# Kernel tuning notes

Hardware: AMD Instinct MI355X
Metric: run time of the kernel (lower is better)

The kernel has to match this reference:

```python
import jax, jax.numpy as jnp
import numpy as np

B = 16      # number of graphs (equal-sized, batch = repeat(arange(B), N))


def _knn_edges(pos, k, total):
    """Batch-aware kNN graph, torch_geometric knn_graph semantics.

    loop=False, flow='source_to_target': for each query node i, its k nearest
    neighbors j produce edges (row=j neighbor/source, col=i query/target).
    Returns (row, col) as flat global int32 index arrays of length B*N*k.
    """
    N = total // B
    posb = pos.reshape(B, N, -1)                      # [B, N, 3]
    sq = jnp.sum(posb * posb, axis=-1)                # [B, N]
    # squared Euclidean distances, [B, N, N]
    d2 = sq[:, :, None] + sq[:, None, :] - 2.0 * jnp.einsum('bnd,bmd->bnm', posb, posb)
    d2 = jnp.where(jnp.eye(N, dtype=bool)[None], jnp.inf, d2)  # exclude self-loops
    _, nbr = jax.lax.top_k(-d2, k)                    # [B, N, k] local neighbor idx
    offs = (jnp.arange(B, dtype=nbr.dtype) * N)[:, None, None]
    row = (nbr + offs).reshape(-1)                                      # neighbors (sources)
    col = jnp.broadcast_to(jnp.arange(N, dtype=nbr.dtype)[None, :, None] + offs,
                           (B, N, k)).reshape(-1)                       # query nodes (targets)
    return row, col


def reference(x, pos, batch, k):
    total = x.shape[0]
    row, col = _knn_edges(pos, k, total)
    # scatter_mean(x[col], row, dim_size=total): mean of gathered features per row index
    sums = jax.ops.segment_sum(x[col], row, num_segments=total)          # [total, d]
    cnt = jax.ops.segment_sum(jnp.ones(row.shape, x.dtype), row, num_segments=total)
    x_neigh_mean = sums / jnp.maximum(cnt, 1.0)[:, None]                 # empty rows -> 0
    return jnp.sum(jnp.abs(x - x_neigh_mean), axis=-1)                   # L1 norm, [total]


def setup_inputs() -> dict:
    key = jax.random.key(0)
    k1, k2 = jax.random.split(key)
    N = 4096
    x = jax.random.normal(k1, (B * N, 64), dtype=jnp.float32)
    pos = jax.random.normal(k2, (B * N, 3), dtype=jnp.float32)
    batch = jnp.repeat(jnp.arange(B, dtype=jnp.int64), N)
    return {"x": x, "pos": pos, "batch": batch, "k": 10}
```

## Files before the change

kernel.cpp:

```cpp
#include <hip/hip_runtime.h>
#include <stdint.h>

#define NB 16
#define NN 4096
#define KK 10
#define NL 11
#define FD 64
#define TOTAL (NB * NN)
#define NW 8
#define CH 512
#define SOCT 32
#define QG 64
#define WCAP 24
#define WPITCH 25

#define INFF __int_as_float(0x7f800000)

typedef float f2 __attribute__((ext_vector_type(2)));

__device__ __forceinline__ f2 FdP(f2 cx, f2 cy, f2 cz, f2 cq,
                                  f2 vx2, f2 vy2, f2 vz2, f2 sqi2) {
#pragma clang fp contract(fast)
    f2 t = sqi2 + cq;
    t = vx2 * cx + t;
    t = vy2 * cy + t;
    t = vz2 * cz + t;
    return t;
}

__device__ __forceinline__ uint32_t d2exact(float mx, float my, float mz, float sqi,
                                            float cx, float cy, float cz, float cw) {
    float dot = __fadd_rn(__fadd_rn(__fmul_rn(mx, cx), __fmul_rn(my, cy)),
                          __fmul_rn(mz, cz));
    float d2 = __fsub_rn(__fadd_rn(sqi, cw), __fmul_rn(2.0f, dot));
    return __float_as_uint(d2);
}

__global__ __launch_bounds__(256) void prep_kernel(const float* __restrict__ pos,
                                                   float4* __restrict__ pp4,
                                                   int* __restrict__ cnt) {
    const int p = blockIdx.x * 256 + threadIdx.x;
    const float* s = pos + (size_t)p * 6;
    float x0 = s[0], y0 = s[1], z0 = s[2];
    float x1 = s[3], y1 = s[4], z1 = s[5];
    float q0 = __fadd_rn(__fadd_rn(__fmul_rn(x0, x0), __fmul_rn(y0, y0)),
                         __fmul_rn(z0, z0));
    float q1 = __fadd_rn(__fadd_rn(__fmul_rn(x1, x1), __fmul_rn(y1, y1)),
                         __fmul_rn(z1, z1));
    pp4[2 * p + 0] = make_float4(x0, x1, y0, y1);
    pp4[2 * p + 1] = make_float4(z0, z1, q0, q1);
    cnt[2 * p + 0] = 0;
    cnt[2 * p + 1] = 0;
}

__global__ __launch_bounds__(512, 8) void knn_kernel(const float4* __restrict__ pp4,
                                                     int* __restrict__ cnt,
                                                     int* __restrict__ colfix,
                                                     int* __restrict__ nbr) {
    __shared__ uint32_t smem[6400];
    __shared__ float tau_s[QG];
    __shared__ uint32_t qcntw[QG * NW];
    float* listf = (float*)smem;
    uint16_t* pool16 = (uint16_t*)smem;

    const int tid = threadIdx.x;
    const int lane = tid & 63;
    const int w = __builtin_amdgcn_readfirstlane(tid >> 6);
    const int batch = blockIdx.x & 15;
    const int qloc = ((blockIdx.x >> 4) << 6) | lane;
    const int gbase = batch << 12;
    const int gq = gbase + qloc;

    float4 mA = pp4[(gq >> 1) * 2 + 0];
    float4 mB = pp4[(gq >> 1) * 2 + 1];
    const bool hi = (qloc & 1);
    const float mx = hi ? mA.y : mA.x;
    const float my = hi ? mA.w : mA.z;
    const float mz = hi ? mB.y : mB.x;
    const float sqi = hi ? mB.w : mB.z;
    const f2 vx22 = {__fmul_rn(-2.0f, mx), __fmul_rn(-2.0f, mx)};
    const f2 vy22 = {__fmul_rn(-2.0f, my), __fmul_rn(-2.0f, my)};
    const f2 vz22 = {__fmul_rn(-2.0f, mz), __fmul_rn(-2.0f, mz)};
    const f2 sqi22 = {sqi, sqi};

    const f2* __restrict__ cp2 = (const f2*)(pp4 + (size_t)(gbase + w * CH));

#define D8P(cb2)                                                      \
    f2 X0 = (cb2)[0],  Y0 = (cb2)[1],  Z0 = (cb2)[2],  Q0 = (cb2)[3]; \
    f2 X1 = (cb2)[4],  Y1 = (cb2)[5],  Z1 = (cb2)[6],  Q1 = (cb2)[7]; \
    f2 X2 = (cb2)[8],  Y2 = (cb2)[9],  Z2 = (cb2)[10], Q2 = (cb2)[11];\
    f2 X3 = (cb2)[12], Y3 = (cb2)[13], Z3 = (cb2)[14], Q3 = (cb2)[15];\
    f2 e0 = FdP(X0, Y0, Z0, Q0, vx22, vy22, vz22, sqi22);             \
    f2 e1 = FdP(X1, Y1, Z1, Q1, vx22, vy22, vz22, sqi22);             \
    f2 e2 = FdP(X2, Y2, Z2, Q2, vx22, vy22, vz22, sqi22);             \
    f2 e3 = FdP(X3, Y3, Z3, Q3, vx22, vy22, vz22, sqi22);

    float L[NL];
#pragma unroll
    for (int t = 0; t < NL; t++) L[t] = INFF;

#pragma unroll 2
    for (int o = 0; o < SOCT; ++o) {
        const f2* cb2 = cp2 + o * 16;
        D8P(cb2);
        float m = fminf(fminf(fminf(e0.x, e0.y), fminf(e1.x, e1.y)),
                        fminf(fminf(e2.x, e2.y), fminf(e3.x, e3.y)));
#pragma unroll
        for (int t = 0; t < NL - 1; ++t) L[t] = __builtin_amdgcn_fmed3f(L[t], L[t + 1], m);
        L[NL - 1] = fminf(L[NL - 1], m);
    }
#pragma unroll
    for (int t = 0; t < NL; t++) listf[tid * NL + t] = L[t];
    __syncthreads();

    if (tid < QG) {
        int p[NW];
#pragma unroll
        for (int u = 0; u < NW; u++) p[u] = NL - 1;
        float tau = INFF;
        for (int it = 0; it < NL; ++it) {
            float best = INFF;
            int bw = 0;
#pragma unroll
            for (int u = 0; u < NW; u++) {
                float v = (p[u] >= 0) ? listf[((u << 6) | tid) * NL + p[u]] : INFF;
                if (v < best) { best = v; bw = u; }
            }
            p[bw]--;
            tau = best;
        }
        tau_s[tid] = tau;
    }
    __syncthreads();

    const float tau = tau_s[lane] * 1.0001f + 1e-5f;
    const uint32_t cell0 = (uint32_t)((lane * NW + w) * WPITCH);
    uint32_t cpos = cell0;
#pragma unroll 2
    for (int o = 0; o < CH / 8; ++o) {
        const f2* cb2 = cp2 + o * 16;
        D8P(cb2);
        const uint32_t jb = (uint32_t)(w * CH + o * 8);
        bool h0 = e0.x <= tau, h1 = e0.y <= tau, h2 = e1.x <= tau, h3 = e1.y <= tau;
        bool h4 = e2.x <= tau, h5 = e2.y <= tau, h6 = e3.x <= tau, h7 = e3.y <= tau;
#define PUSH(hv, off)                                              \
        if ((hv) && cpos < cell0 + WCAP) {                         \
            pool16[cpos] = (uint16_t)(jb + (off));                 \
            cpos++;                                                \
        }
        if (h0 | h1) { PUSH(h0, 0) PUSH(h1, 1) }
        if (h2 | h3) { PUSH(h2, 2) PUSH(h3, 3) }
        if (h4 | h5) { PUSH(h4, 4) PUSH(h5, 5) }
        if (h6 | h7) { PUSH(h6, 6) PUSH(h7, 7) }
#undef PUSH
    }
    qcntw[lane * NW + w] = cpos - cell0;
    __syncthreads();

    if (tid < QG) {
        uint64_t S[KK];
#pragma unroll
        for (int t = 0; t < KK; t++) S[t] = ~0ull;
#pragma unroll
        for (int u = 0; u < NW; u++) {
            uint32_t c2 = qcntw[tid * NW + u];
            const uint16_t* st = pool16 + (tid * NW + u) * WPITCH;
            for (uint32_t e = 0; e < c2; ++e) {
                uint32_t ix = st[e];
                if (ix == (uint32_t)qloc) continue;
                int g = gbase + (int)ix;
                float4 A = pp4[(g >> 1) * 2 + 0];
                float4 B = pp4[(g >> 1) * 2 + 1];
                bool ch = (ix & 1);
                uint32_t db = d2exact(mx, my, mz, sqi,
                                      ch ? A.y : A.x, ch ? A.w : A.z,
                                      ch ? B.y : B.x, ch ? B.w : B.z);
                uint64_t k64 = ((uint64_t)db << 32) | ix;
                if (k64 < S[0]) {
                    bool sh[KK];
                    sh[0] = true;
#pragma unroll
                    for (int t = 1; t < KK; t++) sh[t] = (k64 < S[t]);
#pragma unroll
                    for (int t = 0; t < KK; t++) {
                        uint64_t vac = sh[t] ? k64 : S[t];
                        S[t] = (t + 1 < KK) ? (sh[t + 1] ? S[t + 1] : vac) : vac;
                    }
                }
            }
        }
#pragma unroll
        for (int t = 0; t < KK; t++) {
            int jl = (int)(S[t] & 0xffffffffu);
            int gj = gbase + jl;
            int p = atomicAdd(&cnt[gj], 1);
            if (colfix) {
                if (p < 64) colfix[(gj << 6) | p] = gq;
            } else {
                nbr[gq * KK + t] = gj;
            }
        }
    }
#undef D8P
}

__global__ __launch_bounds__(256) void out_bucket_kernel(const float4* __restrict__ x4,
                                                         const int* __restrict__ colfix,
                                                         const int* __restrict__ cnt,
                                                         float* __restrict__ out) {
    const int b = blockIdx.x;
    const int g = b & 15;
    const int i = b >> 4;
    const int l = threadIdx.x & 31;
    const int n = (g << 12) | (i << 3) | (threadIdx.x >> 5);
    const int s = l & 15;
    const int half = l >> 4;
    const int c = cnt[n];
    const int cc = (c > 64) ? 64 : c;
    const int4* cf4 = (const int4*)(colfix + ((size_t)n << 6));
    float4 acc = make_float4(0.f, 0.f, 0.f, 0.f);
    for (int eb = half * 4; eb < cc; eb += 8) {
        int4 Q = cf4[eb >> 2];
        float4 v0 = x4[((size_t)Q.x << 4) | s];
        acc.x += v0.x; acc.y += v0.y; acc.z += v0.z; acc.w += v0.w;
        if (eb + 1 < cc) {
            float4 v1 = x4[((size_t)Q.y << 4) | s];
            acc.x += v1.x; acc.y += v1.y; acc.z += v1.z; acc.w += v1.w;
        }
        if (eb + 2 < cc) {
            float4 v2 = x4[((size_t)Q.z << 4) | s];
            acc.x += v2.x; acc.y += v2.y; acc.z += v2.z; acc.w += v2.w;
        }
        if (eb + 3 < cc) {
            float4 v3 = x4[((size_t)Q.w << 4) | s];
            acc.x += v3.x; acc.y += v3.y; acc.z += v3.z; acc.w += v3.w;
        }
    }
    acc.x += __shfl_xor(acc.x, 16, 64);
    acc.y += __shfl_xor(acc.y, 16, 64);
    acc.z += __shfl_xor(acc.z, 16, 64);
    acc.w += __shfl_xor(acc.w, 16, 64);
    const float inv = 1.0f / (float)(c > 1 ? c : 1);
    float4 mn = x4[((size_t)n << 4) | s];
    float v = fabsf(mn.x - acc.x * inv) + fabsf(mn.y - acc.y * inv) +
              fabsf(mn.z - acc.z * inv) + fabsf(mn.w - acc.w * inv);
    v += __shfl_xor(v, 1, 64);
    v += __shfl_xor(v, 2, 64);
    v += __shfl_xor(v, 4, 64);
    v += __shfl_xor(v, 8, 64);
    if (l == 0) out[n] = v;
}

__global__ __launch_bounds__(1024) void scan_kernel(const int* __restrict__ cnt,
                                                    int* __restrict__ offs) {
    __shared__ int lds[1024];
    const int t = threadIdx.x;
    const int base = t * 64;
    int s = 0;
    for (int i = 0; i < 64; i++) s += cnt[base + i];
    lds[t] = s;
    __syncthreads();
    for (int off = 1; off < 1024; off <<= 1) {
        int v = (t >= off) ? lds[t - off] : 0;
        __syncthreads();
        lds[t] += v;
        __syncthreads();
    }
    int run = lds[t] - s;
    for (int i = 0; i < 64; i++) {
        offs[base + i] = run;
        run += cnt[base + i];
    }
}

__global__ __launch_bounds__(256) void fill_kernel(const int* __restrict__ nbr,
                                                   int* __restrict__ offs,
                                                   int* __restrict__ col) {
    const int i = blockIdx.x * 256 + threadIdx.x;
#pragma unroll
    for (int t = 0; t < KK; t++) {
        int j = nbr[i * KK + t];
        int p = atomicAdd(&offs[j], 1);
        col[p] = i;
    }
}

__global__ __launch_bounds__(256) void out_kernel(const float* __restrict__ x,
                                                  const int* __restrict__ col,
                                                  const int* __restrict__ offs_end,
                                                  const int* __restrict__ cnt,
                                                  float* __restrict__ out) {
    const int gtid = blockIdx.x * 256 + threadIdx.x;
    const int n = gtid >> 6;
    const int lane = gtid & 63;
    const int c = cnt[n];
    const int end = offs_end[n];
    const int start = end - c;
    float s = 0.0f;
    for (int e = start; e < end; e++) {
        int i = col[e];
        s += x[(size_t)i * FD + lane];
    }
    float mean = s / (float)(c > 1 ? c : 1);
    float v = fabsf(x[(size_t)n * FD + lane] - mean);
#pragma unroll
    for (int off = 32; off; off >>= 1) v += __shfl_xor(v, off, 64);
    if (lane == 0) out[n] = v;
}

extern "C" void kernel_launch(void* const* d_in, const int* in_sizes, int n_in,
                              void* d_out, int out_size, void* d_ws, size_t ws_size,
                              hipStream_t stream) {
    const float* x = (const float*)d_in[0];
    const float* pos = (const float*)d_in[1];
    float* out = (float*)d_out;

    char* ws = (char*)d_ws;
    float4* pp4 = (float4*)(ws + 0);
    int* cnt = (int*)(ws + 1048576);
    int* colfix = (int*)(ws + 1310720);
    int* nbr = (int*)(ws + 1310720);
    int* offs = (int*)(ws + 3932160);
    int* col = (int*)(ws + 4194304);

    const bool bucket = ws_size >= (size_t)(1310720 + TOTAL * 64 * 4);

    hipLaunchKernelGGL(prep_kernel, dim3(TOTAL / 2 / 256), dim3(256), 0, stream, pos, pp4, cnt);
    hipLaunchKernelGGL(knn_kernel, dim3(TOTAL / QG), dim3(512), 0, stream, pp4, cnt,
                       bucket ? colfix : (int*)nullptr, bucket ? (int*)nullptr : nbr);
    if (bucket) {
        hipLaunchKernelGGL(out_bucket_kernel, dim3(TOTAL * 32 / 256), dim3(256), 0, stream,
                           (const float4*)x, colfix, cnt, out);
    } else {
        hipLaunchKernelGGL(scan_kernel, dim3(1), dim3(1024), 0, stream, cnt, offs);
        hipLaunchKernelGGL(fill_kernel, dim3(TOTAL / 256), dim3(256), 0, stream, nbr, offs, col);
        hipLaunchKernelGGL(out_kernel, dim3(TOTAL * FD / 256), dim3(256), 0, stream,
                           x, col, offs, cnt, out);
    }
}
```

Baseline: 186.2 us.

## Parallelize kNN refinement across all waves with merge-path tree reduction

Previously, after candidate collection, only the first wave (64 threads) rescored every wave's candidate pool and held the top-k list. Now each wave rescores its own candidates and keeps a sorted top-10, and the eight per-wave lists are merged pairwise through shared memory in a rank-based tree (8→4→2→1) before emitting edges. The threshold pass is also made cheaper: it drops sqi from the approximate distance, reduces over groups of 32 candidates with an 8-entry list, and uses a looser absolute/relative tau margin. This adds extra barriers and 64-bit shared-memory traffic, and the coarser threshold may admit more candidates or hit the WCAP cap more often.

Result: faster. 175.0 us (-6.0%).

```diff
diff --git a/kernel.cpp b/kernel.cpp
--- a/kernel.cpp
+++ b/kernel.cpp
@@ -4,25 +4,26 @@
 #define NB 16
 #define NN 4096
 #define KK 10
-#define NL 11
+#define NL 8
+#define NSEL 11
+#define LPITCH 9
 #define FD 64
 #define TOTAL (NB * NN)
 #define NW 8
 #define CH 512
-#define SOCT 32
 #define QG 64
 #define WCAP 24
 #define WPITCH 25
+#define SLOTP 11
 
 #define INFF __int_as_float(0x7f800000)
 
 typedef float f2 __attribute__((ext_vector_type(2)));
 
-__device__ __forceinline__ f2 FdP(f2 cx, f2 cy, f2 cz, f2 cq,
-                                  f2 vx2, f2 vy2, f2 vz2, f2 sqi2) {
+__device__ __forceinline__ f2 FdP3(f2 cx, f2 cy, f2 cz, f2 cq,
+                                   f2 vx2, f2 vy2, f2 vz2) {
 #pragma clang fp contract(fast)
-    f2 t = sqi2 + cq;
-    t = vx2 * cx + t;
+    f2 t = vx2 * cx + cq;
     t = vy2 * cy + t;
     t = vz2 * cz + t;
     return t;
@@ -57,11 +58,11 @@
                                                      int* __restrict__ cnt,
                                                      int* __restrict__ colfix,
                                                      int* __restrict__ nbr) {
-    __shared__ uint32_t smem[6400];
+    __shared__ uint64_t smem8[3200];
     __shared__ float tau_s[QG];
-    __shared__ uint32_t qcntw[QG * NW];
-    float* listf = (float*)smem;
-    uint16_t* pool16 = (uint16_t*)smem;
+    float* listf = (float*)smem8;
+    uint16_t* pool16 = (uint16_t*)smem8;
+    uint64_t* slot = smem8;
 
     const int tid = threadIdx.x;
     const int lane = tid & 63;
@@ -81,7 +82,6 @@
     const f2 vx22 = {__fmul_rn(-2.0f, mx), __fmul_rn(-2.0f, mx)};
     const f2 vy22 = {__fmul_rn(-2.0f, my), __fmul_rn(-2.0f, my)};
     const f2 vz22 = {__fmul_rn(-2.0f, mz), __fmul_rn(-2.0f, mz)};
-    const f2 sqi22 = {sqi, sqi};
 
     const f2* __restrict__ cp2 = (const f2*)(pp4 + (size_t)(gbase + w * CH));
 
@@ -90,27 +90,32 @@
     f2 X1 = (cb2)[4],  Y1 = (cb2)[5],  Z1 = (cb2)[6],  Q1 = (cb2)[7]; \
     f2 X2 = (cb2)[8],  Y2 = (cb2)[9],  Z2 = (cb2)[10], Q2 = (cb2)[11];\
     f2 X3 = (cb2)[12], Y3 = (cb2)[13], Z3 = (cb2)[14], Q3 = (cb2)[15];\
-    f2 e0 = FdP(X0, Y0, Z0, Q0, vx22, vy22, vz22, sqi22);             \
-    f2 e1 = FdP(X1, Y1, Z1, Q1, vx22, vy22, vz22, sqi22);             \
-    f2 e2 = FdP(X2, Y2, Z2, Q2, vx22, vy22, vz22, sqi22);             \
-    f2 e3 = FdP(X3, Y3, Z3, Q3, vx22, vy22, vz22, sqi22);
+    f2 e0 = FdP3(X0, Y0, Z0, Q0, vx22, vy22, vz22);                   \
+    f2 e1 = FdP3(X1, Y1, Z1, Q1, vx22, vy22, vz22);                   \
+    f2 e2 = FdP3(X2, Y2, Z2, Q2, vx22, vy22, vz22);                   \
+    f2 e3 = FdP3(X3, Y3, Z3, Q3, vx22, vy22, vz22);
 
     float L[NL];
 #pragma unroll
     for (int t = 0; t < NL; t++) L[t] = INFF;
 
 #pragma unroll 2
-    for (int o = 0; o < SOCT; ++o) {
-        const f2* cb2 = cp2 + o * 16;
-        D8P(cb2);
-        float m = fminf(fminf(fminf(e0.x, e0.y), fminf(e1.x, e1.y)),
-                        fminf(fminf(e2.x, e2.y), fminf(e3.x, e3.y)));
-#pragma unroll
-        for (int t = 0; t < NL - 1; ++t) L[t] = __builtin_amdgcn_fmed3f(L[t], L[t + 1], m);
-        L[NL - 1] = fminf(L[NL - 1], m);
-    }
-#pragma unroll
-    for (int t = 0; t < NL; t++) listf[tid * NL + t] = L[t];
+    for (int g = 0; g < NL; ++g) {
+        float gm = INFF;
+#pragma unroll
+        for (int s = 0; s < 4; ++s) {
+            const f2* cb2 = cp2 + (g * 4 + s) * 16;
+            D8P(cb2);
+            float m = fminf(fminf(fminf(e0.x, e0.y), fminf(e1.x, e1.y)),
+                            fminf(fminf(e2.x, e2.y), fminf(e3.x, e3.y)));
+            gm = fminf(gm, m);
+        }
+#pragma unroll
+        for (int t = 0; t < NL - 1; ++t) L[t] = __builtin_amdgcn_fmed3f(L[t], L[t + 1], gm);
+        L[NL - 1] = fminf(L[NL - 1], gm);
+    }
+#pragma unroll
+    for (int t = 0; t < NL; t++) listf[tid * LPITCH + t] = L[t];
     __syncthreads();
 
     if (tid < QG) {
@@ -118,12 +123,12 @@
 #pragma unroll
         for (int u = 0; u < NW; u++) p[u] = NL - 1;
         float tau = INFF;
-        for (int it = 0; it < NL; ++it) {
+        for (int it = 0; it < NSEL; ++it) {
             float best = INFF;
             int bw = 0;
 #pragma unroll
             for (int u = 0; u < NW; u++) {
-                float v = (p[u] >= 0) ? listf[((u << 6) | tid) * NL + p[u]] : INFF;
+                float v = (p[u] >= 0) ? listf[((u << 6) | tid) * LPITCH + p[u]] : INFF;
                 if (v < best) { best = v; bw = u; }
             }
             p[bw]--;
@@ -133,8 +138,9 @@
     }
     __syncthreads();
 
-    const float tau = tau_s[lane] * 1.0001f + 1e-5f;
-    const uint32_t cell0 = (uint32_t)((lane * NW + w) * WPITCH);
+    const float t0v = tau_s[lane];
+    const float tau = t0v + fabsf(t0v) * 1e-4f + 1e-4f;
+    const uint32_t cell0 = (uint32_t)(((w << 6) | lane) * WPITCH);
     uint32_t cpos = cell0;
 #pragma unroll 2
     for (int o = 0; o < CH / 8; ++o) {
@@ -154,52 +160,129 @@
         if (h6 | h7) { PUSH(h6, 6) PUSH(h7, 7) }
 #undef PUSH
     }
-    qcntw[lane * NW + w] = cpos - cell0;
-    __syncthreads();
-
-    if (tid < QG) {
-        uint64_t S[KK];
-#pragma unroll
-        for (int t = 0; t < KK; t++) S[t] = ~0ull;
-#pragma unroll
-        for (int u = 0; u < NW; u++) {
-            uint32_t c2 = qcntw[tid * NW + u];
-            const uint16_t* st = pool16 + (tid * NW + u) * WPITCH;
-            for (uint32_t e = 0; e < c2; ++e) {
-                uint32_t ix = st[e];
-                if (ix == (uint32_t)qloc) continue;
-                int g = gbase + (int)ix;
-                float4 A = pp4[(g >> 1) * 2 + 0];
-                float4 B = pp4[(g >> 1) * 2 + 1];
-                bool ch = (ix & 1);
-                uint32_t db = d2exact(mx, my, mz, sqi,
-                                      ch ? A.y : A.x, ch ? A.w : A.z,
-                                      ch ? B.y : B.x, ch ? B.w : B.z);
-                uint64_t k64 = ((uint64_t)db << 32) | ix;
-                if (k64 < S[0]) {
-                    bool sh[KK];
-                    sh[0] = true;
-#pragma unroll
-                    for (int t = 1; t < KK; t++) sh[t] = (k64 < S[t]);
-#pragma unroll
-                    for (int t = 0; t < KK; t++) {
-                        uint64_t vac = sh[t] ? k64 : S[t];
-                        S[t] = (t + 1 < KK) ? (sh[t + 1] ? S[t + 1] : vac) : vac;
-                    }
+
+    uint64_t S[KK];
+#pragma unroll
+    for (int t = 0; t < KK; t++) S[t] = ~0ull;
+    {
+        const uint16_t* st = pool16 + cell0;
+        const int c2i = (int)(cpos - cell0);
+        for (int e = 0; e < c2i; ++e) {
+            uint32_t ix = st[e];
+            if (ix == (uint32_t)qloc) continue;
+            int g = gbase + (int)ix;
+            float4 A4 = pp4[(g >> 1) * 2 + 0];
+            float4 B4 = pp4[(g >> 1) * 2 + 1];
+            bool ch = (ix & 1);
+            uint32_t db = d2exact(mx, my, mz, sqi,
+                                  ch ? A4.y : A4.x, ch ? A4.w : A4.z,
+                                  ch ? B4.y : B4.x, ch ? B4.w : B4.z);
+            uint64_t k64 = ((uint64_t)db << 32) | ix;
+            if (k64 < S[0]) {
+                bool sh[KK];
+                sh[0] = true;
+#pragma unroll
+                for (int t = 1; t < KK; t++) sh[t] = (k64 < S[t]);
+#pragma unroll
+                for (int t = 0; t < KK; t++) {
+                    uint64_t vac = sh[t] ? k64 : S[t];
+                    S[t] = (t + 1 < KK) ? (sh[t + 1] ? S[t + 1] : vac) : vac;
                 }
             }
         }
-#pragma unroll
-        for (int t = 0; t < KK; t++) {
-            int jl = (int)(S[t] & 0xffffffffu);
-            int gj = gbase + jl;
-            int p = atomicAdd(&cnt[gj], 1);
-            if (colfix) {
-                if (p < 64) colfix[(gj << 6) | p] = gq;
-            } else {
-                nbr[gq * KK + t] = gj;
-            }
-        }
+    }
+    __syncthreads();
+
+    if (w >= 4) {
+        uint64_t* sl = slot + (((w - 4) << 6) | lane) * SLOTP;
+#pragma unroll
+        for (int j = 0; j < KK; ++j) sl[j] = S[KK - 1 - j];
+    }
+    __syncthreads();
+
+    if (w < 4) {
+        uint64_t* sl = slot + ((w << 6) | lane) * SLOTP;
+        uint64_t P[KK];
+#pragma unroll
+        for (int j = 0; j < KK; ++j) P[j] = sl[j];
+#pragma unroll
+        for (int j = 0; j < KK; ++j) {
+            uint64_t v = S[KK - 1 - j];
+            uint32_t r = (uint32_t)j;
+#pragma unroll
+            for (int i = 0; i < KK; ++i) r += (P[i] < v) ? 1u : 0u;
+            if (r < KK) sl[r] = v;
+        }
+#pragma unroll
+        for (int i = 0; i < KK; ++i) {
+            uint64_t v = P[i];
+            uint32_t r = (uint32_t)i;
+#pragma unroll
+            for (int t = 0; t < KK; ++t) r += (S[t] <= v) ? 1u : 0u;
+            if (r < KK) sl[r] = v;
+        }
+    }
+    __syncthreads();
+
+    if (w < 2) {
+        uint64_t* sa = slot + (((w * 2) << 6) | lane) * SLOTP;
+        uint64_t* sb = slot + (((w * 2 + 1) << 6) | lane) * SLOTP;
+        uint64_t Aa[KK], Bb[KK];
+#pragma unroll
+        for (int j = 0; j < KK; ++j) Aa[j] = sa[j];
+#pragma unroll
+        for (int j = 0; j < KK; ++j) Bb[j] = sb[j];
+#pragma unroll
+        for (int j = 0; j < KK; ++j) {
+            uint32_t r = (uint32_t)j;
+#pragma unroll
+            for (int i = 0; i < KK; ++i) r += (Bb[i] < Aa[j]) ? 1u : 0u;
+            if (r < KK) sa[r] = Aa[j];
+        }
+#pragma unroll
+        for (int i = 0; i < KK; ++i) {
+            uint32_t r = (uint32_t)i;
+#pragma unroll
+            for (int j = 0; j < KK; ++j) r += (Aa[j] <= Bb[i]) ? 1u : 0u;
+            if (r < KK) sa[r] = Bb[i];
+        }
+    }
+    __syncthreads();
+
+    if (tid < QG) {
+        const uint64_t* sa = slot + ((0 << 6) | tid) * SLOTP;
+        const uint64_t* sb = slot + ((2 << 6) | tid) * SLOTP;
+        uint64_t Aa[KK], Bb[KK];
+#pragma unroll
+        for (int j = 0; j < KK; ++j) Aa[j] = sa[j];
+#pragma unroll
+        for (int j = 0; j < KK; ++j) Bb[j] = sb[j];
+#define EMIT(key, rk)                                              \
+        {                                                          \
+            int jl = (int)((key) & 0xffffffffu);                   \
+            int gj = gbase + jl;                                   \
+            int p = atomicAdd(&cnt[gj], 1);                        \
+            if (colfix) {                                          \
+                if (p < 64) colfix[(gj << 6) | p] = gq;            \
+            } else {                                               \
+                nbr[gq * KK + (int)(rk)] = gj;                     \
+            }                                                      \
+        }
+#pragma unroll
+        for (int j = 0; j < KK; ++j) {
+            uint32_t r = (uint32_t)j;
+#pragma unroll
+            for (int i = 0; i < KK; ++i) r += (Bb[i] < Aa[j]) ? 1u : 0u;
+            if (r < KK) EMIT(Aa[j], r)
+        }
+#pragma unroll
+        for (int i = 0; i < KK; ++i) {
+            uint32_t r = (uint32_t)i;
+#pragma unroll
+            for (int j = 0; j < KK; ++j) r += (Aa[j] <= Bb[i]) ? 1u : 0u;
+            if (r < KK) EMIT(Bb[i], r)
+        }
+#undef EMIT
     }
 #undef D8P
 }
```
